# Kernel optimization log

Hardware: AMD Instinct MI355X
Metric: run time of the kernel (lower is better)

Reference implementation:

```python
import jax, jax.numpy as jnp
import numpy as np

B, D, K, P = 512, 2048, 128, 5

def setup_inputs() -> dict:
    key = jax.random.key(0)
    k1, k2 = jax.random.split(key)
    x = jax.random.normal(k1, (B, D), dtype=jnp.float32)
    theta = 0.05 * jax.random.normal(k2, (D, K, P), dtype=jnp.float32)
    log_weight_scale = jnp.zeros((K, P), dtype=jnp.float32)
    bias = -jnp.ones((K,), dtype=jnp.float32)  # layer inits bias to -1
    return {"x": x, "theta": theta, "log_weight_scale": log_weight_scale, "bias": bias}

def reference(x, theta, log_weight_scale, bias):
    b = x.shape[0]
    # weight-normalized kernel: [D, K, P]
    norm = jnp.sqrt(jnp.sum(theta * theta, axis=0))            # [K, P]
    kernel = theta * (jnp.exp(log_weight_scale) / norm)[None]  # [D, K, P]
    actv = jnp.einsum('bd,dkp->bkp', x, kernel)                # [B, K, P]
    # pairwise L1 over P: [B, K, B]
    diff = jnp.abs(actv[:, :, :, None] - jnp.transpose(actv, (1, 2, 0))[None])  # [B,K,P,B]
    abs_dif = jnp.sum(diff, axis=2) + 1e6 * jnp.eye(b, dtype=x.dtype)[:, None, :]
    f = jnp.sum(jnp.exp(-abs_dif), axis=2) + bias[None, :]     # [B, K]
    return jnp.concatenate([x, f], axis=1)                     # [B, D+K]
```

## Files before the change

kernel.cpp:

```cpp
#include <hip/hip_runtime.h>
#include <math.h>

#define BSZ 512
#define DD 2048
#define KK 128
#define PP 5
#define NCOL (KK * PP)
#define OUTW (DD + KK)
#define LOG2E 1.4426950408889634f

#define KSPLIT 16
#define GK (DD / KSPLIT)

typedef __attribute__((ext_vector_type(8))) short bf16x8;
typedef __attribute__((ext_vector_type(4))) float f32x4;

#define WS_NORM 0
#define WS_ACTV (WS_NORM + NCOL)
#define WS_XB (WS_ACTV + BSZ * NCOL)
#define WS_THT (WS_XB + BSZ * DD / 2)
#define WS_PART (WS_THT + NCOL * DD / 2)

__device__ inline ushort f2b(float f) {
    unsigned u = __float_as_uint(f);
    u += 0x7FFF + ((u >> 16) & 1);
    return (ushort)(u >> 16);
}

#define SWZ(r, c) ((((r) * 128) + ((c) ^ (((r) & 7) << 3))))

__global__ __launch_bounds__(256) void prep_kernel(const float* __restrict__ theta,
                                                   const float* __restrict__ x,
                                                   float* __restrict__ norm,
                                                   ushort* __restrict__ thT,
                                                   ushort* __restrict__ xb) {
    __shared__ float partial[32][8];
    __shared__ ushort sT[64][68];

    const int bid = blockIdx.x;
    const int t   = threadIdx.x;

    if (bid < 80) {
        const int c8  = bid * 8;
        const int col = c8 + (t & 7);
        const int g   = t >> 3;
        const float* p = theta + (size_t)g * NCOL + col;
        float s = 0.f;
#pragma unroll
        for (int j = 0; j < 64; ++j) {
            float v = p[(size_t)j * 32 * NCOL];
            s += v * v;
        }
        partial[g][t & 7] = s;
        __syncthreads();
        if (t < 8) {
            float acc = 0.f;
#pragma unroll
            for (int gg = 0; gg < 32; ++gg) acc += partial[gg][t];
            norm[c8 + t] = acc;
        }
    } else if (bid < 400) {
        const int tb    = bid - 80;
        const int kz    = (tb & 31) * 64;
        const int nz    = (tb >> 5) * 64;
        const int c4    = t & 15;
        const int rbase = t >> 4;
#pragma unroll
        for (int i = 0; i < 4; ++i) {
            int r = rbase + i * 16;
            float4 v = *(const float4*)&theta[(size_t)(kz + r) * NCOL + nz + c4 * 4];
            sT[c4 * 4 + 0][r] = f2b(v.x);
            sT[c4 * 4 + 1][r] = f2b(v.y);
            sT[c4 * 4 + 2][r] = f2b(v.z);
            sT[c4 * 4 + 3][r] = f2b(v.w);
        }
        __syncthreads();
#pragma unroll
        for (int i = 0; i < 2; ++i) {
            int slot = t + i * 256;
            int rr   = slot >> 3;
            int cc   = (slot & 7) * 8;
            ushort4 w0 = *(const ushort4*)&sT[rr][cc];
            ushort4 w1 = *(const ushort4*)&sT[rr][cc + 4];
            ushort* dst = &thT[(size_t)(nz + rr) * DD + kz + cc];
            *(ushort4*)&dst[0] = w0;
            *(ushort4*)&dst[4] = w1;
        }
    } else {
        const int b2 = bid - 400;
#pragma unroll
        for (int i = 0; i < 4; ++i) {
            int base = b2 * 4096 + i * 1024 + t * 4;
            float4 v = *(const float4*)&x[base];
            ushort4 w;
            w.x = f2b(v.x); w.y = f2b(v.y); w.z = f2b(v.z); w.w = f2b(v.w);
            *(ushort4*)&xb[base] = w;
        }
    }
}

__global__ __launch_bounds__(256) void gemm_kernel(const ushort* __restrict__ xb,
                                                   const ushort* __restrict__ thT,
                                                   ushort* __restrict__ parth,
                                                   const float* __restrict__ x,
                                                   float* __restrict__ out) {
    __shared__ ushort lA[64 * 128];
    __shared__ ushort lB[64 * 128];

    const int bx = blockIdx.x;
    if (bx >= 1280) {
        const int bid = bx - 1280;
        for (int i = bid * 256 + threadIdx.x; i < BSZ * (DD / 4); i += 80 * 256) {
            int r = i >> 9;
            int c = i & 511;
            float4 v = *(const float4*)&x[(size_t)r * DD + c * 4];
            *(float4*)&out[(size_t)r * OUTW + c * 4] = v;
        }
        return;
    }

    const int t    = threadIdx.x;
    const int lane = t & 63;
    const int wave = t >> 6;
    const int mt8  = bx & 7;
    const int rest = bx >> 3;
    const int bn   = (rest % 10) * 64;
    const int bm   = mt8 * 64;
    const int z    = rest / 10;
    const int kz   = z * GK;

    const ushort* gA = xb  + (size_t)bm * DD + kz;
    const ushort* gB = thT + (size_t)bn * DD + kz;

    const int srr = t >> 4;
    const int sss = t & 15;

    uint4 va[4], vb[4];
#pragma unroll
    for (int i = 0; i < 4; ++i) {
        int rr = srr + i * 16;
        va[i] = *(const uint4*)&gA[(size_t)rr * DD + sss * 8];
        vb[i] = *(const uint4*)&gB[(size_t)rr * DD + sss * 8];
    }
#pragma unroll
    for (int i = 0; i < 4; ++i) {
        int rr = srr + i * 16;
        *(uint4*)&lA[SWZ(rr, sss * 8)] = va[i];
        *(uint4*)&lB[SWZ(rr, sss * 8)] = vb[i];
    }
    __syncthreads();

    const int fr = lane & 15;
    const int g  = lane >> 4;
    const int mr = (wave >> 1) * 32 + fr;
    const int nr = (wave & 1) * 32 + fr;

    f32x4 acc[2][2] = {};
#pragma unroll
    for (int ks = 0; ks < 4; ++ks) {
        const int kc = ks * 32 + g * 8;
        bf16x8 a0 = *(const bf16x8*)&lA[SWZ(mr,      kc)];
        bf16x8 a1 = *(const bf16x8*)&lA[SWZ(mr + 16, kc)];
        bf16x8 b0 = *(const bf16x8*)&lB[SWZ(nr,      kc)];
        bf16x8 b1 = *(const bf16x8*)&lB[SWZ(nr + 16, kc)];
        acc[0][0] = __builtin_amdgcn_mfma_f32_16x16x32_bf16(a0, b0, acc[0][0], 0, 0, 0);
        acc[0][1] = __builtin_amdgcn_mfma_f32_16x16x32_bf16(a0, b1, acc[0][1], 0, 0, 0);
        acc[1][0] = __builtin_amdgcn_mfma_f32_16x16x32_bf16(a1, b0, acc[1][0], 0, 0, 0);
        acc[1][1] = __builtin_amdgcn_mfma_f32_16x16x32_bf16(a1, b1, acc[1][1], 0, 0, 0);
    }

    ushort* base = parth + (size_t)z * (BSZ * NCOL);
#pragma unroll
    for (int mt = 0; mt < 2; ++mt)
#pragma unroll
        for (int nt = 0; nt < 2; ++nt) {
            int row = bm + (wave >> 1) * 32 + mt * 16 + g * 4;
            int col = bn + (wave & 1) * 32 + nt * 16 + fr;
            ushort* dst = base + (size_t)row * NCOL + col;
#pragma unroll
            for (int reg = 0; reg < 4; ++reg)
                dst[(size_t)reg * NCOL] = f2b(acc[mt][nt][reg]);
        }
}

__global__ __launch_bounds__(256) void reduce_kernel(const ushort* __restrict__ parth,
                                                     const float* __restrict__ norm,
                                                     const float* __restrict__ lws,
                                                     float* __restrict__ actv) {
    int i   = (blockIdx.x * 256 + threadIdx.x) * 2;
    int b   = i / NCOL;
    int col = i - b * NCOL;
    float s0 = 0.f, s1 = 0.f;
#pragma unroll
    for (int q = 0; q < KSPLIT; ++q) {
        unsigned u = *(const unsigned*)&parth[(size_t)q * (BSZ * NCOL) + i];
        s0 += __uint_as_float(u << 16);
        s1 += __uint_as_float(u & 0xffff0000u);
    }
    const float sc0 = __builtin_amdgcn_exp2f(lws[col] * LOG2E) *
                      __builtin_amdgcn_rsqf(norm[col]) * LOG2E;
    const float sc1 = __builtin_amdgcn_exp2f(lws[col + 1] * LOG2E) *
                      __builtin_amdgcn_rsqf(norm[col + 1]) * LOG2E;
    int k0 = col / 5,       p0 = col - k0 * 5;
    int k1 = (col + 1) / 5, p1 = (col + 1) - k1 * 5;
    actv[((size_t)k0 * BSZ + b) * PP + p0] = s0 * sc0;
    actv[((size_t)k1 * BSZ + b) * PP + p1] = s1 * sc1;
}

__global__ __launch_bounds__(512) void pairwise_kernel(const float* __restrict__ actv,
                                                       const float* __restrict__ bias,
                                                       float* __restrict__ out) {
    const int k    = blockIdx.x;
    const int rc   = blockIdx.y;
    const int tid  = threadIdx.x;
    const int lane = tid & 63;
    const int seg  = tid >> 6;

    __shared__ float sB[512][8];
    __shared__ float red[8][256];

    const float* col = actv + (size_t)k * (BSZ * PP);
    for (int i = tid; i < BSZ * PP; i += 512) {
        int rr = i / 5;
        sB[rr][i - rr * 5] = col[i];
    }
    __syncthreads();

    const int r0 = rc * 256 + lane;
    float a[4][PP];
#pragma unroll
    for (int r = 0; r < 4; ++r)
#pragma unroll
        for (int p = 0; p < PP; ++p)
            a[r][p] = sB[r0 + r * 64][p];

    float acc[4] = {0.f, 0.f, 0.f, 0.f};
    const int j0 = seg * 64;
#pragma unroll 4
    for (int jj = 0; jj < 64; ++jj) {
        const float4 v  = *(const float4*)&sB[j0 + jj][0];
        const float  v4 = sB[j0 + jj][4];
#pragma unroll
        for (int r = 0; r < 4; ++r) {
            float s = fabsf(a[r][0] - v.x) + fabsf(a[r][1] - v.y) +
                      fabsf(a[r][2] - v.z) + fabsf(a[r][3] - v.w) +
                      fabsf(a[r][4] - v4);
            acc[r] += __builtin_amdgcn_exp2f(-s);
        }
    }
#pragma unroll
    for (int r = 0; r < 4; ++r)
        red[seg][lane + r * 64] = acc[r];
    __syncthreads();

    if (tid < 256) {
        float s = red[0][tid] + red[1][tid] + red[2][tid] + red[3][tid] +
                  red[4][tid] + red[5][tid] + red[6][tid] + red[7][tid];
        out[(size_t)(rc * 256 + tid) * OUTW + DD + k] = s - 1.0f + bias[k];
    }
}

extern "C" void kernel_launch(void* const* d_in, const int* in_sizes, int n_in,
                              void* d_out, int out_size, void* d_ws, size_t ws_size,
                              hipStream_t stream) {
    const float* x     = (const float*)d_in[0];
    const float* theta = (const float*)d_in[1];
    const float* lws   = (const float*)d_in[2];
    const float* bias  = (const float*)d_in[3];
    float* out = (float*)d_out;

    float* ws     = (float*)d_ws;
    float* norm   = ws + WS_NORM;
    float* actv   = ws + WS_ACTV;
    ushort* xb    = (ushort*)(ws + WS_XB);
    ushort* thT   = (ushort*)(ws + WS_THT);
    ushort* parth = (ushort*)(ws + WS_PART);

    prep_kernel<<<656, 256, 0, stream>>>(theta, x, norm, thT, xb);
    gemm_kernel<<<1360, 256, 0, stream>>>(xb, thT, parth, x, out);
    reduce_kernel<<<640, 256, 0, stream>>>(parth, norm, lws, actv);
    pairwise_kernel<<<dim3(KK, 2), 512, 0, stream>>>(actv, bias, out);
}
```

Baseline: 100.1 us.

## Fuse split-K reduction and scaling into pairwise kernel, store partials in k-major layout

The GEMM epilogue now writes bf16 split-K partials in a [z][k][b][p] layout, so each pairwise block can load its k-slice contiguously. The separate reduce kernel is removed: pairwise blocks sum the 16 partials in shared memory and apply the exp(lws)/norm scale themselves. This saves one kernel launch and the fp32 actv round trip through global memory. In exchange, the GEMM stores become more scattered, each of the 2 row-chunk blocks redundantly reduces the partials, and shared memory per block grows by about 80KB, which may limit occupancy.

After: 114.7 us. 14.6% more time.

```diff
diff --git a/kernel.cpp b/kernel.cpp
--- a/kernel.cpp
+++ b/kernel.cpp
@@ -16,8 +16,7 @@
 typedef __attribute__((ext_vector_type(4))) float f32x4;
 
 #define WS_NORM 0
-#define WS_ACTV (WS_NORM + NCOL)
-#define WS_XB (WS_ACTV + BSZ * NCOL)
+#define WS_XB (WS_NORM + NCOL)
 #define WS_THT (WS_XB + BSZ * DD / 2)
 #define WS_PART (WS_THT + NCOL * DD / 2)
 
@@ -25,6 +24,9 @@
     unsigned u = __float_as_uint(f);
     u += 0x7FFF + ((u >> 16) & 1);
     return (ushort)(u >> 16);
+}
+__device__ inline float b2f(ushort h) {
+    return __uint_as_float((unsigned)h << 16);
 }
 
 #define SWZ(r, c) ((((r) * 128) + ((c) ^ (((r) & 7) << 3))))
@@ -169,45 +171,24 @@
         acc[1][1] = __builtin_amdgcn_mfma_f32_16x16x32_bf16(a1, b1, acc[1][1], 0, 0, 0);
     }
 
-    ushort* base = parth + (size_t)z * (BSZ * NCOL);
 #pragma unroll
     for (int mt = 0; mt < 2; ++mt)
 #pragma unroll
         for (int nt = 0; nt < 2; ++nt) {
             int row = bm + (wave >> 1) * 32 + mt * 16 + g * 4;
             int col = bn + (wave & 1) * 32 + nt * 16 + fr;
-            ushort* dst = base + (size_t)row * NCOL + col;
+            int kq  = col / 5;
+            int p   = col - kq * 5;
+            ushort* dst = parth + ((size_t)(z * KK + kq) * BSZ + row) * PP + p;
 #pragma unroll
             for (int reg = 0; reg < 4; ++reg)
-                dst[(size_t)reg * NCOL] = f2b(acc[mt][nt][reg]);
-        }
-}
-
-__global__ __launch_bounds__(256) void reduce_kernel(const ushort* __restrict__ parth,
-                                                     const float* __restrict__ norm,
-                                                     const float* __restrict__ lws,
-                                                     float* __restrict__ actv) {
-    int i   = (blockIdx.x * 256 + threadIdx.x) * 2;
-    int b   = i / NCOL;
-    int col = i - b * NCOL;
-    float s0 = 0.f, s1 = 0.f;
-#pragma unroll
-    for (int q = 0; q < KSPLIT; ++q) {
-        unsigned u = *(const unsigned*)&parth[(size_t)q * (BSZ * NCOL) + i];
-        s0 += __uint_as_float(u << 16);
-        s1 += __uint_as_float(u & 0xffff0000u);
-    }
-    const float sc0 = __builtin_amdgcn_exp2f(lws[col] * LOG2E) *
-                      __builtin_amdgcn_rsqf(norm[col]) * LOG2E;
-    const float sc1 = __builtin_amdgcn_exp2f(lws[col + 1] * LOG2E) *
-                      __builtin_amdgcn_rsqf(norm[col + 1]) * LOG2E;
-    int k0 = col / 5,       p0 = col - k0 * 5;
-    int k1 = (col + 1) / 5, p1 = (col + 1) - k1 * 5;
-    actv[((size_t)k0 * BSZ + b) * PP + p0] = s0 * sc0;
-    actv[((size_t)k1 * BSZ + b) * PP + p1] = s1 * sc1;
-}
-
-__global__ __launch_bounds__(512) void pairwise_kernel(const float* __restrict__ actv,
+                dst[(size_t)reg * PP] = f2b(acc[mt][nt][reg]);
+        }
+}
+
+__global__ __launch_bounds__(512) void pairwise_kernel(const ushort* __restrict__ parth,
+                                                       const float* __restrict__ norm,
+                                                       const float* __restrict__ lws,
                                                        const float* __restrict__ bias,
                                                        float* __restrict__ out) {
     const int k    = blockIdx.x;
@@ -216,13 +197,39 @@
     const int lane = tid & 63;
     const int seg  = tid >> 6;
 
+    __shared__ unsigned raw[KSPLIT * 1280];
     __shared__ float sB[512][8];
     __shared__ float red[8][256];
 
-    const float* col = actv + (size_t)k * (BSZ * PP);
-    for (int i = tid; i < BSZ * PP; i += 512) {
-        int rr = i / 5;
-        sB[rr][i - rr * 5] = col[i];
+    const unsigned* g = (const unsigned*)parth + (size_t)k * 1280;
+#pragma unroll
+    for (int q = 0; q < KSPLIT; ++q) {
+        const unsigned* gq = g + (size_t)q * (KK * 1280);
+#pragma unroll
+        for (int s = 0; s < 3; ++s) {
+            int idx = s * 512 + tid;
+            if (idx < 1280) raw[q * 1280 + idx] = gq[idx];
+        }
+    }
+    __syncthreads();
+
+    {
+        const ushort* rawU = (const ushort*)raw;
+        const int b = tid;
+        float s[PP] = {};
+#pragma unroll
+        for (int q = 0; q < KSPLIT; ++q) {
+            int o = q * 2560 + 5 * b;
+#pragma unroll
+            for (int p = 0; p < PP; ++p) s[p] += b2f(rawU[o + p]);
+        }
+#pragma unroll
+        for (int p = 0; p < PP; ++p) {
+            int col = k * PP + p;
+            float sc = __builtin_amdgcn_exp2f(lws[col] * LOG2E) *
+                       __builtin_amdgcn_rsqf(norm[col]) * LOG2E;
+            sB[b][p] = s[p] * sc;
+        }
     }
     __syncthreads();
 
@@ -271,13 +278,11 @@
 
     float* ws     = (float*)d_ws;
     float* norm   = ws + WS_NORM;
-    float* actv   = ws + WS_ACTV;
     ushort* xb    = (ushort*)(ws + WS_XB);
     ushort* thT   = (ushort*)(ws + WS_THT);
     ushort* parth = (ushort*)(ws + WS_PART);
 
     prep_kernel<<<656, 256, 0, stream>>>(theta, x, norm, thT, xb);
     gemm_kernel<<<1360, 256, 0, stream>>>(xb, thT, parth, x, out);
-    reduce_kernel<<<640, 256, 0, stream>>>(parth, norm, lws, actv);
-    pairwise_kernel<<<dim3(KK, 2), 512, 0, stream>>>(actv, bias, out);
-}
+    pairwise_kernel<<<dim3(KK, 2), 512, 0, stream>>>(parth, norm, lws, bias, out);
+}
```
